# Kernel optimization log

Measured on AMD Instinct MI355X. Metric: run time of the kernel, lower is better.

## Reference

```python
import jax, jax.numpy as jnp
import numpy as np
import math

B, T, C, H, D, R = 1, 2048, 2048, 16, 128, 64
W_LOCAL = 512
DELTA_I = 0.75
ROPE_BASE = 10000.0


def _rotate(x):
    # interleaved rotate-half, exactly as in the torch source
    x1, x2 = x[..., ::2], x[..., 1::2]
    return jnp.stack((-x2, x1), axis=-1).reshape(x.shape)


def _rope_tables(seq_len):
    inv_freq = 1.0 / (ROPE_BASE ** (jnp.arange(0, D, 2, dtype=jnp.float32) / D))
    t = jnp.arange(seq_len, dtype=jnp.float32)
    freqs = jnp.einsum('i,j->ij', t, inv_freq)          # [T, D/2]
    emb = jnp.concatenate((freqs, freqs), axis=-1)      # [T, D] (half-layout, as in source)
    return jnp.cos(emb)[None, None], jnp.sin(emb)[None, None]


def setup_inputs() -> dict:
    key = jax.random.key(0)
    ks = jax.random.split(key, 8)
    s = 0.02
    return {
        'x': jax.random.normal(ks[0], (B, T, C), dtype=jnp.float32),
        'w_qkv': jax.random.normal(ks[1], (3 * C, C), dtype=jnp.float32) * s,
        'w_o': jax.random.normal(ks[2], (C, C), dtype=jnp.float32) * s,
        'pk': jax.random.normal(ks[3], (R, D), dtype=jnp.float32) * s,
        'pv': jax.random.normal(ks[4], (R, D), dtype=jnp.float32) * s,
        'uo': jax.random.normal(ks[5], (D, R), dtype=jnp.float32) * s,
        'info_w1': jax.random.normal(ks[6], (C // 4, C), dtype=jnp.float32) * s,
        'info_w2': jax.random.normal(ks[7], (1, C // 4), dtype=jnp.float32) * s,
    }


def reference(x, w_qkv, w_o, pk, pv, uo, info_w1, info_w2):
    Bx, Tx, Cx = x.shape
    scale = 1.0 / math.sqrt(D)

    qkv = x @ w_qkv.T                                   # [B,T,3C]
    q, k, v = jnp.split(qkv, 3, axis=-1)
    q = q.reshape(Bx, Tx, H, D).transpose(0, 2, 1, 3)   # [B,H,T,D]
    k = k.reshape(Bx, Tx, H, D).transpose(0, 2, 1, 3)
    v = v.reshape(Bx, Tx, H, D).transpose(0, 2, 1, 3)

    cos, sin = _rope_tables(Tx)
    q = q * cos + _rotate(q) * sin
    k = k * cos + _rotate(k) * sin

    # causal local-window attention (full [B,H,T,T] scores, as in source)
    w = min(W_LOCAL, Tx)
    idx = jnp.arange(Tx)
    rel = idx[None, :] - idx[:, None]                   # j - i
    local_mask = (rel > 0) | (rel < -(w - 1))           # True = masked
    scores = jnp.einsum('bhtd,bhsd->bhts', q, k) * scale
    scores = jnp.where(local_mask[None, None], -jnp.inf, scores)
    attn_local = jax.nn.softmax(scores, axis=-1)
    ctx_local = jnp.einsum('bhts,bhsd->bhtd', attn_local, v)

    # informational gate (no-grad path in source)
    h_info = jax.nn.gelu(x @ info_w1.T, approximate=False)
    info_score = jax.nn.sigmoid((h_info @ info_w2.T)[..., 0])   # [B,T]
    gate = (info_score > DELTA_I).astype(x.dtype)

    # low-rank global path (unmasked softmax over all tokens, as in source)
    k_r = jnp.einsum('bhsd,rd->bhsr', k, pk)
    v_r = jnp.einsum('bhsd,rd->bhsr', v, pv)
    q_r = jnp.einsum('bhtd,rd->bhtr', q, pk)
    scores_g = jnp.einsum('bhtr,bhsr->bhts', q_r, k_r) * (scale * D / R)
    attn_g = jax.nn.softmax(scores_g, axis=-1)
    ctx_g_r = jnp.einsum('bhts,bhsr->bhtr', attn_g, v_r)
    ctx_g = jnp.einsum('bhtr,dr->bhtd', ctx_g_r, uo)
    gate_q = gate[:, None, :, None]                     # [B,1,T,1]
    ctx = ctx_local + ctx_g * gate_q

    ctx = ctx.transpose(0, 2, 1, 3).reshape(Bx, Tx, Cx)
    return ctx @ w_o.T
```

## Files before the change

### kernel.cpp

```cpp
#include <hip/hip_runtime.h>
#include <hip/hip_bf16.h>
#include <math.h>

#define T_LEN 2048
#define C_DIM 2048
#define NH 16
#define HD 128
#define RANK 64
#define W_LOCAL 512
#define QKV_LD 6144
#define ROW_BF 12288
#define KB_OFF 4096
#define VB_OFF 8192
#define WO_OFF 6144
#define SCALE 0.08838834764831845f
#define SCALE_G 0.17677669529663687f
#define LOG1E4_OVER_64 0.14391156831212787f

typedef __bf16 bf16_t;
typedef __bf16 bf16x8 __attribute__((ext_vector_type(8)));
typedef __bf16 bf16x4 __attribute__((ext_vector_type(4)));
typedef float f32x4 __attribute__((ext_vector_type(4)));

__device__ __forceinline__ void async_copy16(const bf16_t* g, bf16_t* l) {
    __builtin_amdgcn_global_load_lds(
        (const __attribute__((address_space(1))) unsigned int*)g,
        (__attribute__((address_space(3))) unsigned int*)l, 16, 0, 0);
}

__global__ __launch_bounds__(256)
void prep_kernel(const float* __restrict__ x, bf16_t* __restrict__ xb,
                 const float* __restrict__ w_qkv, bf16_t* __restrict__ wqb,
                 float* __restrict__ tab) {
    const int bid = blockIdx.x;
    const int tid = threadIdx.x;
    if (bid < 2048) {
        int idx = bid * 256 + tid;
        const float* p = x + (size_t)idx * 8;
        float4 v0 = *(const float4*)p;
        float4 v1 = *(const float4*)(p + 4);
        bf16x8 o;
        o[0] = (bf16_t)v0.x; o[1] = (bf16_t)v0.y; o[2] = (bf16_t)v0.z; o[3] = (bf16_t)v0.w;
        o[4] = (bf16_t)v1.x; o[5] = (bf16_t)v1.y; o[6] = (bf16_t)v1.z; o[7] = (bf16_t)v1.w;
        *(bf16x8*)(xb + (size_t)idx * 8) = o;
    } else if (bid < 8192) {
        int idx = (bid - 2048) * 256 + tid;
        const float* p = w_qkv + (size_t)idx * 8;
        float4 v0 = *(const float4*)p;
        float4 v1 = *(const float4*)(p + 4);
        bf16x8 o;
        o[0] = (bf16_t)v0.x; o[1] = (bf16_t)v0.y; o[2] = (bf16_t)v0.z; o[3] = (bf16_t)v0.w;
        o[4] = (bf16_t)v1.x; o[5] = (bf16_t)v1.y; o[6] = (bf16_t)v1.z; o[7] = (bf16_t)v1.w;
        *(bf16x8*)(wqb + (size_t)idx * 8) = o;
    } else {
        int idx = (bid - 8192) * 256 + tid;
        int t = idx >> 6, j = idx & 63;
        float inv = expf(-(float)j * LOG1E4_OVER_64);
        float s, c;
        sincosf((float)t * inv, &s, &c);
        tab[t * 128 + j] = c;
        tab[t * 128 + 64 + j] = s;
    }
}

#define NTK 32
#define ILD 40

#define STG_A(bb, ktile) do {                                                  \
    _Pragma("unroll")                                                          \
    for (int c_ = 0; c_ < 4; ++c_)                                             \
        async_copy16(gA + (size_t)(c_ * 32) * 2048 + (ktile) * 64,             \
                     &lds[bb][0][(c_ * 32 + rS) * 64 + dS]);                   \
} while (0)

#define STG_B(bb, ktile) do {                                                  \
    _Pragma("unroll")                                                          \
    for (int c_ = 0; c_ < 4; ++c_)                                             \
        async_copy16(gB + (size_t)(c_ * 32) * 2048 + (ktile) * 64,             \
                     &lds[bb][1][(c_ * 32 + rS) * 64 + dS]);                   \
} while (0)

#define RD_A(bb, m, k) (*(const bf16x8*)&lds[bb][0][(wr * 64 + (m) * 16 + l16) * 64 + (((k) * 4 + quad) ^ xsw) * 8])
#define RD_B(bb, n, k) (*(const bf16x8*)&lds[bb][1][(wc * 64 + (n) * 16 + l16) * 64 + (((k) * 4 + quad) ^ xsw) * 8])

__global__ __launch_bounds__(256, 2)
void gemm_qkv_rope(const bf16_t* __restrict__ A, const bf16_t* __restrict__ B,
                   bf16_t* __restrict__ qkv_bf, bf16_t* __restrict__ vt,
                   const float* __restrict__ tab, const float* __restrict__ w_o,
                   const float* __restrict__ x, const float* __restrict__ w1,
                   float* __restrict__ ipart) {
    __shared__ __align__(16) unsigned char smem[65536];
    const int bid = blockIdx.x;
    const int tid = threadIdx.x;

    if (bid < 128) {
        bf16_t* Ah = (bf16_t*)smem;
        bf16_t* Al = Ah + 128 * ILD;
        bf16_t* Bh = Al + 128 * ILD;
        bf16_t* Bl = Bh + 128 * ILD;
        const int bn = bid & 3, bm = (bid >> 2) & 15, ks = bid >> 6;
        const int wave = tid >> 6, lane = tid & 63;
        const int quad = lane >> 4, l16 = lane & 15;
        const int wm = (wave >> 1) * 64, wn = (wave & 1) * 64;
        const int lrow = lane >> 2;
        const int lkb = (lane & 3) * 8;
        const int kbeg = ks * 1024;

        f32x4 acc[4][4];
#pragma unroll
        for (int i = 0; i < 4; ++i)
#pragma unroll
            for (int j = 0; j < 4; ++j) acc[i][j] = (f32x4){0.f, 0.f, 0.f, 0.f};

        const float* gx = x + (size_t)(bm * 128 + wave * 16 + lrow) * 2048 + kbeg + lkb;
        const float* gw = w1 + (size_t)(bn * 128 + wave * 16 + lrow) * 2048 + kbeg + lkb;
        const int wrow = (wave * 16 + lrow) * ILD + lkb;

        for (int k0 = 0; k0 < 1024; k0 += 32) {
            __syncthreads();
#pragma unroll
            for (int hr = 0; hr < 2; ++hr) {
                const float* px = gx + (size_t)hr * 64 * 2048 + k0;
                float4 a0 = *(const float4*)px, a1 = *(const float4*)(px + 4);
                float av[8] = {a0.x, a0.y, a0.z, a0.w, a1.x, a1.y, a1.z, a1.w};
                bf16x8 h, l;
#pragma unroll
                for (int i = 0; i < 8; ++i) {
                    bf16_t hb = (bf16_t)av[i];
                    h[i] = hb; l[i] = (bf16_t)(av[i] - (float)hb);
                }
                *(bf16x8*)&Ah[wrow + hr * 64 * ILD] = h;
                *(bf16x8*)&Al[wrow + hr * 64 * ILD] = l;

                const float* pw = gw + (size_t)hr * 64 * 2048 + k0;
                float4 b0 = *(const float4*)pw, b1 = *(const float4*)(pw + 4);
                float bv[8] = {b0.x, b0.y, b0.z, b0.w, b1.x, b1.y, b1.z, b1.w};
                bf16x8 hb2, lb2;
#pragma unroll
                for (int i = 0; i < 8; ++i) {
                    bf16_t hh = (bf16_t)bv[i];
                    hb2[i] = hh; lb2[i] = (bf16_t)(bv[i] - (float)hh);
                }
                *(bf16x8*)&Bh[wrow + hr * 64 * ILD] = hb2;
                *(bf16x8*)&Bl[wrow + hr * 64 * ILD] = lb2;
            }
            __syncthreads();

            bf16x8 ah[4], al[4], bh[4], bl[4];
#pragma unroll
            for (int mt = 0; mt < 4; ++mt) {
                ah[mt] = *(const bf16x8*)&Ah[(wm + mt * 16 + l16) * ILD + quad * 8];
                al[mt] = *(const bf16x8*)&Al[(wm + mt * 16 + l16) * ILD + quad * 8];
            }
#pragma unroll
            for (int nt = 0; nt < 4; ++nt) {
                bh[nt] = *(const bf16x8*)&Bh[(wn + nt * 16 + l16) * ILD + quad * 8];
                bl[nt] = *(const bf16x8*)&Bl[(wn + nt * 16 + l16) * ILD + quad * 8];
            }
#pragma unroll
            for (int mt = 0; mt < 4; ++mt)
#pragma unroll
                for (int nt = 0; nt < 4; ++nt) {
                    acc[mt][nt] = __builtin_amdgcn_mfma_f32_16x16x32_bf16(ah[mt], bh[nt], acc[mt][nt], 0, 0, 0);
                    acc[mt][nt] = __builtin_amdgcn_mfma_f32_16x16x32_bf16(ah[mt], bl[nt], acc[mt][nt], 0, 0, 0);
                    acc[mt][nt] = __builtin_amdgcn_mfma_f32_16x16x32_bf16(al[mt], bh[nt], acc[mt][nt], 0, 0, 0);
                }
        }

        float* cp = ipart + (size_t)ks * 2048 * 512;
#pragma unroll
        for (int mt = 0; mt < 4; ++mt)
#pragma unroll
            for (int r = 0; r < 4; ++r) {
                int row = bm * 128 + wm + mt * 16 + quad * 4 + r;
                float* crow = cp + (size_t)row * 512 + bn * 128 + wn;
#pragma unroll
                for (int nt = 0; nt < 4; ++nt)
                    crow[nt * 16 + l16] = acc[mt][nt][r];
            }
        return;
    }

    if (bid >= 896) {
        int row = bid - 896;
        int c = tid * 8;
        const float* p = w_o + (size_t)row * 2048 + c;
        float4 v0 = *(const float4*)p;
        float4 v1 = *(const float4*)(p + 4);
        bf16x8 o;
        o[0] = (bf16_t)v0.x; o[1] = (bf16_t)v0.y; o[2] = (bf16_t)v0.z; o[3] = (bf16_t)v0.w;
        o[4] = (bf16_t)v1.x; o[5] = (bf16_t)v1.y; o[6] = (bf16_t)v1.z; o[7] = (bf16_t)v1.w;
        *(bf16x8*)(qkv_bf + (size_t)row * ROW_BF + WO_OFF + c) = o;
        return;
    }

    typedef bf16_t ldsbuf_t[2][128 * 64];
    ldsbuf_t* lds = (ldsbuf_t*)smem;

    const int gid = bid - 128;
    const int xcd = gid & 7, idx = gid >> 3;
    const int bn_ = xcd * 6 + (idx >> 4);
    const int bm_ = idx & 15;
    const int wave = tid >> 6, lane = tid & 63;
    const int quad = lane >> 4, l16 = lane & 15;
    const int wr = wave >> 1, wc = wave & 1;
    const int xsw = l16 & 7;

    const int rS = tid >> 3;
    const int cS = ((tid & 7) ^ (rS & 7)) * 8;
    const int dS = (tid & 7) * 8;
    const bf16_t* gA = A + (size_t)(bm_ * 128 + rS) * 2048 + cS;
    const bf16_t* gB = B + (size_t)(bn_ * 128 + rS) * 2048 + cS;

    f32x4 acc[4][4];
#pragma unroll
    for (int i = 0; i < 4; ++i)
#pragma unroll
        for (int j = 0; j < 4; ++j) acc[i][j] = (f32x4){0.f, 0.f, 0.f, 0.f};

    STG_A(0, 0); STG_B(0, 0);
    STG_A(1, 1); STG_B(1, 1);
    asm volatile("s_waitcnt vmcnt(8)" ::: "memory");
    __builtin_amdgcn_s_barrier();

    for (int kt = 0; kt < NTK; ++kt) {
        const int b = kt & 1;
        bf16x8 af[4][2], bfr[4][2];
#pragma unroll
        for (int m = 0; m < 4; ++m) { af[m][0] = RD_A(b, m, 0); af[m][1] = RD_A(b, m, 1); }
#pragma unroll
        for (int n = 0; n < 4; ++n) { bfr[n][0] = RD_B(b, n, 0); bfr[n][1] = RD_B(b, n, 1); }
        asm volatile("s_waitcnt lgkmcnt(0)" ::: "memory");
        __builtin_amdgcn_s_barrier();

        __builtin_amdgcn_s_setprio(1);
#pragma unroll
        for (int m = 0; m < 4; ++m)
#pragma unroll
            for (int n = 0; n < 4; ++n)
                acc[m][n] = __builtin_amdgcn_mfma_f32_16x16x32_bf16(af[m][0], bfr[n][0], acc[m][n], 0, 0, 0);
        __builtin_amdgcn_s_setprio(0);
        if (kt + 2 < NTK) STG_A(b, kt + 2);

        __builtin_amdgcn_s_setprio(1);
#pragma unroll
        for (int m = 0; m < 4; ++m)
#pragma unroll
            for (int n = 0; n < 4; ++n)
                acc[m][n] = __builtin_amdgcn_mfma_f32_16x16x32_bf16(af[m][1], bfr[n][1], acc[m][n], 0, 0, 0);
        __builtin_amdgcn_s_setprio(0);
        if (kt + 2 < NTK) STG_B(b, kt + 2);

        if (kt < NTK - 2) { asm volatile("s_waitcnt vmcnt(8)" ::: "memory"); }
        else              { asm volatile("s_waitcnt vmcnt(0)" ::: "memory"); }
        __builtin_amdgcn_s_barrier();
    }

    const int colbase = bn_ * 128 + wc * 64;
    const int region = (bn_ * 128) >> 11;
    const int rowbase = bm_ * 128 + wr * 64;
    const bool odd = (l16 & 1);

    if (region == 2) {
#pragma unroll
        for (int mt = 0; mt < 4; ++mt)
#pragma unroll
            for (int r = 0; r < 4; ++r) {
                int t = rowbase + mt * 16 + quad * 4 + r;
                bf16_t* brow = qkv_bf + (size_t)t * ROW_BF + VB_OFF + (colbase - 4096);
#pragma unroll
                for (int nt = 0; nt < 4; ++nt)
                    brow[nt * 16 + l16] = (bf16_t)acc[mt][nt][r];
            }
        bf16_t* Tl = (bf16_t*)smem;
#pragma unroll
        for (int mt = 0; mt < 4; ++mt)
#pragma unroll
            for (int r = 0; r < 4; ++r) {
                int rloc = wr * 64 + mt * 16 + quad * 4 + r;
#pragma unroll
                for (int nt = 0; nt < 4; ++nt) {
                    int cloc = wc * 64 + nt * 16 + l16;
                    Tl[cloc * 136 + rloc] = (bf16_t)acc[mt][nt][r];
                }
            }
        __syncthreads();
        const int hh = bn_ - 32;
        const int d = tid >> 1, th = (tid & 1) * 64;
        bf16_t* dst = vt + ((size_t)(hh * 128 + d)) * 2048 + bm_ * 128 + th;
        const bf16_t* srcT = Tl + d * 136 + th;
#pragma unroll
        for (int j = 0; j < 8; ++j)
            *(bf16x8*)(dst + j * 8) = *(const bf16x8*)(srcT + j * 8);
    } else {
#pragma unroll
        for (int mt = 0; mt < 4; ++mt)
#pragma unroll
            for (int r = 0; r < 4; ++r) {
                int t = rowbase + mt * 16 + quad * 4 + r;
                const float* trow = tab + t * 128;
#pragma unroll
                for (int nt = 0; nt < 4; ++nt) {
                    float v = acc[mt][nt][r];
                    float vp = __shfl_xor(v, 1);
                    int col = colbase + nt * 16 + l16;
                    int j = col & 63;
                    float c = trow[j], s = trow[64 + j];
                    float y = odd ? (v * c + vp * s) : (v * c - vp * s);
                    qkv_bf[(size_t)t * ROW_BF + (region == 0 ? col : col + 2048)] = (bf16_t)y;
                }
            }
    }
}

#define STG_A2(bb, ktile) do {                                                 \
    _Pragma("unroll")                                                          \
    for (int c_ = 0; c_ < 4; ++c_)                                             \
        async_copy16(gA + (size_t)(c_ * 32) * 2048 + (ktile) * 64,             \
                     &lds[bb][0][(c_ * 32 + rS) * 64 + dS]);                   \
} while (0)

#define STG_B2(bb, ktile) do {                                                 \
    _Pragma("unroll")                                                          \
    for (int c_ = 0; c_ < 4; ++c_)                                             \
        async_copy16(gB + (size_t)(c_ * 32) * ROW_BF + (ktile) * 64,           \
                     &lds[bb][1][(c_ * 32 + rS) * 64 + dS]);                   \
} while (0)

__global__ __launch_bounds__(256, 2)
void gemm_ctx_wo(const bf16_t* __restrict__ A, const bf16_t* __restrict__ Bov,
                 float* __restrict__ C) {
    __shared__ __align__(16) bf16_t ldss[2][2][128 * 64];
    typedef bf16_t ldsbuf_t[2][128 * 64];
    ldsbuf_t* lds = (ldsbuf_t*)ldss;

    const int bid = blockIdx.x;
    const int xcd = bid & 7, idx = bid >> 3;
    const int bn_ = xcd * 2 + (idx >> 4);
    const int bm_ = idx & 15;
    const int tid = threadIdx.x;
    const int wave = tid >> 6, lane = tid & 63;
    const int quad = lane >> 4, l16 = lane & 15;
    const int wr = wave >> 1, wc = wave & 1;
    const int xsw = l16 & 7;

    const int rS = tid >> 3;
    const int cS = ((tid & 7) ^ (rS & 7)) * 8;
    const int dS = (tid & 7) * 8;
    const bf16_t* gA = A + (size_t)(bm_ * 128 + rS) * 2048 + cS;
    const bf16_t* gB = Bov + (size_t)(bn_ * 128 + rS) * ROW_BF + cS;

    f32x4 acc[4][4];
#pragma unroll
    for (int i = 0; i < 4; ++i)
#pragma unroll
        for (int j = 0; j < 4; ++j) acc[i][j] = (f32x4){0.f, 0.f, 0.f, 0.f};

    STG_A2(0, 0); STG_B2(0, 0);
    STG_A2(1, 1); STG_B2(1, 1);
    asm volatile("s_waitcnt vmcnt(8)" ::: "memory");
    __builtin_amdgcn_s_barrier();

    for (int kt = 0; kt < NTK; ++kt) {
        const int b = kt & 1;
        bf16x8 af[4][2], bfr[4][2];
#pragma unroll
        for (int m = 0; m < 4; ++m) { af[m][0] = RD_A(b, m, 0); af[m][1] = RD_A(b, m, 1); }
#pragma unroll
        for (int n = 0; n < 4; ++n) { bfr[n][0] = RD_B(b, n, 0); bfr[n][1] = RD_B(b, n, 1); }
        asm volatile("s_waitcnt lgkmcnt(0)" ::: "memory");
        __builtin_amdgcn_s_barrier();

        __builtin_amdgcn_s_setprio(1);
#pragma unroll
        for (int m = 0; m < 4; ++m)
#pragma unroll
            for (int n = 0; n < 4; ++n)
                acc[m][n] = __builtin_amdgcn_mfma_f32_16x16x32_bf16(af[m][0], bfr[n][0], acc[m][n], 0, 0, 0);
        __builtin_amdgcn_s_setprio(0);
        if (kt + 2 < NTK) STG_A2(b, kt + 2);

        __builtin_amdgcn_s_setprio(1);
#pragma unroll
        for (int m = 0; m < 4; ++m)
#pragma unroll
            for (int n = 0; n < 4; ++n)
                acc[m][n] = __builtin_amdgcn_mfma_f32_16x16x32_bf16(af[m][1], bfr[n][1], acc[m][n], 0, 0, 0);
        __builtin_amdgcn_s_setprio(0);
        if (kt + 2 < NTK) STG_B2(b, kt + 2);

        if (kt < NTK - 2) { asm volatile("s_waitcnt vmcnt(8)" ::: "memory"); }
        else              { asm volatile("s_waitcnt vmcnt(0)" ::: "memory"); }
        __builtin_amdgcn_s_barrier();
    }

    const int colbase = bn_ * 128 + wc * 64;
    const int rowbase = bm_ * 128 + wr * 64;
#pragma unroll
    for (int mt = 0; mt < 4; ++mt)
#pragma unroll
        for (int r = 0; r < 4; ++r) {
            int row = rowbase + mt * 16 + quad * 4 + r;
            float* crow = C + (size_t)row * 2048 + colbase;
#pragma unroll
            for (int nt = 0; nt < 4; ++nt)
                crow[nt * 16 + l16] = acc[mt][nt][r];
        }
}

__device__ __forceinline__ float gelu_exact(float v) {
    return 0.5f * v * (1.0f + erff(v * 0.70710678118654752f));
}

__global__ __launch_bounds__(64)
void info_gate_kernel(const float* __restrict__ Cpart, const float* __restrict__ w2,
                      float* __restrict__ gate) {
    const int t = blockIdx.x;
    const int lane = threadIdx.x;
    const float* p0 = Cpart + (size_t)t * 512;
    float s = 0.f;
#pragma unroll
    for (int i = lane; i < 512; i += 64) {
        float v = p0[i] + p0[i + 1048576];
        s += gelu_exact(v) * w2[i];
    }
#pragma unroll
    for (int off = 32; off > 0; off >>= 1) s += __shfl_down(s, off);
    if (lane == 0) {
        float sig = 1.f / (1.f + expf(-s));
        gate[t] = (sig > 0.75f) ? 1.f : 0.f;
    }
}

#define KV_LD 136

__global__ __launch_bounds__(256)
void kvr_mfma_kernel(const bf16_t* __restrict__ qkv_bf,
                     const float* __restrict__ pk, const float* __restrict__ pv,
                     float* __restrict__ kr, float* __restrict__ vr,
                     bf16_t* __restrict__ qr) {
    __shared__ bf16_t Kt[64 * KV_LD];
    __shared__ bf16_t Vt[64 * KV_LD];
    __shared__ bf16_t Qt[64 * KV_LD];
    __shared__ bf16_t Pk[64 * KV_LD];
    __shared__ bf16_t Pv[64 * KV_LD];

    const int h = blockIdx.y;
    const int s0 = blockIdx.x * 64;
    const int tid = threadIdx.x;
    const int wave = tid >> 6, lane = tid & 63;
    const int quad = lane >> 4, l16 = lane & 15;

#pragma unroll
    for (int i = 0; i < 4; ++i) {
        int gid = i * 256 + tid;
        int row = gid >> 4, ch = (gid & 15) << 3;
        const bf16_t* rb = qkv_bf + (size_t)(s0 + row) * ROW_BF + h * HD + ch;
        *(bf16x8*)&Qt[row * KV_LD + ch] = *(const bf16x8*)(rb);
        *(bf16x8*)&Kt[row * KV_LD + ch] = *(const bf16x8*)(rb + KB_OFF);
        *(bf16x8*)&Vt[row * KV_LD + ch] = *(const bf16x8*)(rb + VB_OFF);
    }
#pragma unroll
    for (int i = 0; i < 8; ++i) {
        int gid = i * 256 + tid;
        int row = gid >> 5, c = (gid & 31) << 2;
        float4 wk = *(const float4*)(pk + (size_t)row * HD + c);
        float4 wv = *(const float4*)(pv + (size_t)row * HD + c);
        bf16x4 qk4, qv4;
        qk4[0] = (bf16_t)wk.x; qk4[1] = (bf16_t)wk.y; qk4[2] = (bf16_t)wk.z; qk4[3] = (bf16_t)wk.w;
        qv4[0] = (bf16_t)wv.x; qv4[1] = (bf16_t)wv.y; qv4[2] = (bf16_t)wv.z; qv4[3] = (bf16_t)wv.w;
        *(bf16x4*)&Pk[row * KV_LD + c] = qk4;
        *(bf16x4*)&Pv[row * KV_LD + c] = qv4;
    }
    __syncthreads();

    f32x4 ak[4], av[4], aq[4];
#pragma unroll
    for (int nt = 0; nt < 4; ++nt) {
        ak[nt] = (f32x4){0.f, 0.f, 0.f, 0.f};
        av[nt] = (f32x4){0.f, 0.f, 0.f, 0.f};
        aq[nt] = (f32x4){0.f, 0.f, 0.f, 0.f};
    }

#pragma unroll
    for (int ks = 0; ks < 4; ++ks) {
        const int ao = (wave * 16 + l16) * KV_LD + ks * 32 + quad * 8;
        bf16x8 a_k = *(const bf16x8*)&Kt[ao];
        bf16x8 a_v = *(const bf16x8*)&Vt[ao];
        bf16x8 a_q = *(const bf16x8*)&Qt[ao];
#pragma unroll
        for (int nt = 0; nt < 4; ++nt) {
            const int bo = (nt * 16 + l16) * KV_LD + ks * 32 + quad * 8;
            bf16x8 bk = *(const bf16x8*)&Pk[bo];
            bf16x8 bv = *(const bf16x8*)&Pv[bo];
            ak[nt] = __builtin_amdgcn_mfma_f32_16x16x32_bf16(a_k, bk, ak[nt], 0, 0, 0);
            av[nt] = __builtin_amdgcn_mfma_f32_16x16x32_bf16(a_v, bv, av[nt], 0, 0, 0);
            aq[nt] = __builtin_amdgcn_mfma_f32_16x16x32_bf16(a_q, bk, aq[nt], 0, 0, 0);
        }
    }

#pragma unroll
    for (int nt = 0; nt < 4; ++nt)
#pragma unroll
        for (int r = 0; r < 4; ++r) {
            int s = s0 + wave * 16 + quad * 4 + r;
            size_t idx = ((size_t)h * T_LEN + s) * RANK + nt * 16 + l16;
            kr[idx] = ak[nt][r];
            vr[idx] = av[nt][r];
            qr[idx] = (bf16_t)aq[nt][r];
        }
}

#define QTI 64
#define KTI 64
#define PS_LD 72

__global__ __launch_bounds__(256)
void local_attn_kernel(const bf16_t* __restrict__ qkv_bf, const bf16_t* __restrict__ vt,
                       bf16_t* __restrict__ cxb) {
    __shared__ __align__(16) bf16_t Qs[QTI * 128];
    __shared__ __align__(16) bf16_t Ks[KTI * 128];
    __shared__ __align__(16) bf16_t Vts[128 * KTI];
    __shared__ bf16_t Ps[4][16 * PS_LD];

    const int h = blockIdx.y;
    const int t0 = blockIdx.x * QTI;
    const int tid = threadIdx.x;
    const int wave = tid >> 6, lane = tid & 63;
    const int quad = lane >> 4, l16 = lane & 15;
    const int xsw = l16 & 7;

    const bf16_t* vth = vt + (size_t)h * 128 * 2048;

#pragma unroll
    for (int i = 0; i < 4; ++i) {
        int c = i * 256 + tid;
        int row = c >> 4, pc = c & 15;
        int lc = pc ^ (row & 7);
        async_copy16(qkv_bf + (size_t)(t0 + row) * ROW_BF + h * HD + lc * 8, &Qs[c * 8]);
    }

    f32x4 o[8];
#pragma unroll
    for (int d8 = 0; d8 < 8; ++d8) o[d8] = (f32x4){0.f, 0.f, 0.f, 0.f};
    float m_i[4] = {-1e30f, -1e30f, -1e30f, -1e30f};
    float l_i[4] = {0.f, 0.f, 0.f, 0.f};

    __syncthreads();

    for (int kt = 0; kt < 9; ++kt) {
        const int sbase = t0 - 512 + kt * KTI;
        if (sbase < 0) continue;
        __syncthreads();
#pragma unroll
        for (int i = 0; i < 4; ++i) {
            int c = i * 256 + tid;
            int row = c >> 4, pc = c & 15;
            int lc = pc ^ (row & 7);
            async_copy16(qkv_bf + (size_t)(sbase + row) * ROW_BF + KB_OFF + h * HD + lc * 8,
                         &Ks[c * 8]);
        }
#pragma unroll
        for (int i = 0; i < 4; ++i) {
            int c = i * 256 + tid;
            int row = c >> 3, pc = c & 7;
            int lc = pc ^ (row & 7);
            async_copy16(vth + (size_t)row * 2048 + sbase + lc * 8, &Vts[c * 8]);
        }
        __syncthreads();

        f32x4 sacc[4];
#pragma unroll
        for (int nt = 0; nt < 4; ++nt) sacc[nt] = (f32x4){0.f, 0.f, 0.f, 0.f};
#pragma unroll
        for (int ks = 0; ks < 4; ++ks) {
            bf16x8 a = *(const bf16x8*)&Qs[(wave * 16 + l16) * 128 + (((ks * 4 + quad) ^ xsw)) * 8];
#pragma unroll
            for (int nt = 0; nt < 4; ++nt) {
                bf16x8 b = *(const bf16x8*)&Ks[(nt * 16 + l16) * 128 + (((ks * 4 + quad) ^ xsw)) * 8];
                sacc[nt] = __builtin_amdgcn_mfma_f32_16x16x32_bf16(a, b, sacc[nt], 0, 0, 0);
            }
        }

#pragma unroll
        for (int nt = 0; nt < 4; ++nt)
#pragma unroll
            for (int r = 0; r < 4; ++r) sacc[nt][r] *= SCALE;

        if (kt == 0 || kt == 8) {
#pragma unroll
            for (int nt = 0; nt < 4; ++nt) {
                int s_g = sbase + nt * 16 + l16;
#pragma unroll
                for (int r = 0; r < 4; ++r) {
                    int t_g = t0 + wave * 16 + quad * 4 + r;
                    bool valid = (s_g <= t_g) && (s_g + W_LOCAL > t_g);
                    if (!valid) sacc[nt][r] = -1e30f;
                }
            }
        }

#pragma unroll
        for (int r = 0; r < 4; ++r) {
            float mx = fmaxf(fmaxf(sacc[0][r], sacc[1][r]), fmaxf(sacc[2][r], sacc[3][r]));
            mx = fmaxf(mx, __shfl_xor(mx, 1));
            mx = fmaxf(mx, __shfl_xor(mx, 2));
            mx = fmaxf(mx, __shfl_xor(mx, 4));
            mx = fmaxf(mx, __shfl_xor(mx, 8));
            float mnew = fmaxf(m_i[r], mx);
            float alpha = __expf(m_i[r] - mnew);
            m_i[r] = mnew;
            float rs = 0.f;
#pragma unroll
            for (int nt = 0; nt < 4; ++nt) {
                float p = __expf(sacc[nt][r] - mnew);
                sacc[nt][r] = p;
                rs += p;
            }
            rs += __shfl_xor(rs, 1);
            rs += __shfl_xor(rs, 2);
            rs += __shfl_xor(rs, 4);
            rs += __shfl_xor(rs, 8);
            l_i[r] = l_i[r] * alpha + rs;
#pragma unroll
            for (int d8 = 0; d8 < 8; ++d8) o[d8][r] *= alpha;
        }

#pragma unroll
        for (int r = 0; r < 4; ++r)
#pragma unroll
            for (int nt = 0; nt < 4; ++nt)
                Ps[wave][(quad * 4 + r) * PS_LD + nt * 16 + l16] = (bf16_t)sacc[nt][r];

#pragma unroll
        for (int ks2 = 0; ks2 < 2; ++ks2) {
            bf16x8 a = *(const bf16x8*)&Ps[wave][l16 * PS_LD + ks2 * 32 + quad * 8];
#pragma unroll
            for (int d8 = 0; d8 < 8; ++d8) {
                int rw = d8 * 16 + l16;
                bf16x8 b = *(const bf16x8*)&Vts[rw * 64 + (((ks2 * 4 + quad) ^ xsw)) * 8];
                o[d8] = __builtin_amdgcn_mfma_f32_16x16x32_bf16(a, b, o[d8], 0, 0, 0);
            }
        }
    }

#pragma unroll
    for (int r = 0; r < 4; ++r) {
        float inv = 1.0f / l_i[r];
        size_t rowoff = (size_t)(t0 + wave * 16 + quad * 4 + r) * 2048 + h * HD;
#pragma unroll
        for (int d8 = 0; d8 < 8; ++d8)
            cxb[rowoff + d8 * 16 + l16] = (bf16_t)(o[d8][r] * inv);
    }
}

__device__ __forceinline__ float block_reduce_max512(float v, float* red, int tid) {
    red[tid] = v; __syncthreads();
    for (int s = 256; s > 0; s >>= 1) {
        if (tid < s) red[tid] = fmaxf(red[tid], red[tid + s]);
        __syncthreads();
    }
    float r = red[0]; __syncthreads();
    return r;
}
__device__ __forceinline__ float block_reduce_sum512(float v, float* red, int tid) {
    red[tid] = v; __syncthreads();
    for (int s = 256; s > 0; s >>= 1) {
        if (tid < s) red[tid] = red[tid] + red[tid + s];
        __syncthreads();
    }
    float r = red[0]; __syncthreads();
    return r;
}

__global__ __launch_bounds__(512)
void global_attn_kernel(bf16_t* __restrict__ cxb, const float* __restrict__ kr,
                        const float* __restrict__ vr, const bf16_t* __restrict__ qr,
                        const float* __restrict__ uo, const float* __restrict__ gate) {
    const int t = blockIdx.x, h = blockIdx.y;
    if (gate[t] <= 0.5f) return;

    __shared__ float qrs[64];
    __shared__ float red[512];
    __shared__ float cgr[64];
    __shared__ float sg[2048];
    const int tid = threadIdx.x;

    if (tid < 64) qrs[tid] = (float)qr[((size_t)h * T_LEN + t) * RANK + tid];
    __syncthreads();

    const float* krh = kr + (size_t)h * T_LEN * RANK;
    const float* vrh = vr + (size_t)h * T_LEN * RANK;
    float lmax = -INFINITY;
    for (int s = tid; s < T_LEN; s += 512) {
        const float* krr = krh + (size_t)s * RANK;
        float acc = 0.f;
#pragma unroll
        for (int r = 0; r < RANK; r += 4) {
            float4 k4 = *(const float4*)(krr + r);
            acc += qrs[r] * k4.x + qrs[r + 1] * k4.y + qrs[r + 2] * k4.z + qrs[r + 3] * k4.w;
        }
        float sc = acc * SCALE_G;
        sg[s] = sc;
        lmax = fmaxf(lmax, sc);
    }
    float gmx = block_reduce_max512(lmax, red, tid);
    float lsum = 0.f;
    for (int s = tid; s < T_LEN; s += 512) {
        float pp = expf(sg[s] - gmx);
        sg[s] = pp;
        lsum += pp;
    }
    float gsum = block_reduce_sum512(lsum, red, tid);

    {
        const int r = tid & 63, part = tid >> 6;
        float pacc = 0.f;
        for (int s = part; s < T_LEN; s += 8) pacc += sg[s] * vrh[(size_t)s * RANK + r];
        red[tid] = pacc;
        __syncthreads();
        if (tid < 64) {
            float c = 0.f;
#pragma unroll
            for (int pp = 0; pp < 8; ++pp) c += red[pp * 64 + tid];
            cgr[tid] = c / gsum;
        }
        __syncthreads();
    }

    if (tid < 128) {
        float cg = 0.f;
#pragma unroll
        for (int r = 0; r < RANK; ++r) cg += cgr[r] * uo[tid * RANK + r];
        size_t off = (size_t)t * 2048 + h * HD + tid;
        cxb[off] = (bf16_t)((float)cxb[off] + cg);
    }
}

extern "C" void kernel_launch(void* const* d_in, const int* in_sizes, int n_in,
                              void* d_out, int out_size, void* d_ws, size_t ws_size,
                              hipStream_t stream) {
    const float* x     = (const float*)d_in[0];
    const float* w_qkv = (const float*)d_in[1];
    const float* w_o   = (const float*)d_in[2];
    const float* pk    = (const float*)d_in[3];
    const float* pv    = (const float*)d_in[4];
    const float* uo    = (const float*)d_in[5];
    const float* w1    = (const float*)d_in[6];
    const float* w2    = (const float*)d_in[7];
    float* out = (float*)d_out;

    float* ws = (float*)d_ws;
    float* qkv   = ws;
    float* hinfo = qkv + (size_t)12582912;
    float* gatep = hinfo + (size_t)1048576;
    bf16_t* xb   = (bf16_t*)(gatep + 2048);
    float* wqbf  = gatep + 2048 + 2097152;
    bf16_t* wqb  = (bf16_t*)wqbf;
    float* krp   = wqbf;
    float* vrp   = wqbf + (size_t)2097152;
    float* tabp  = hinfo;
    bf16_t* qrp  = (bf16_t*)hinfo;
    bf16_t* cxb  = xb;
    bf16_t* qkvb = (bf16_t*)qkv;
    bf16_t* wob  = qkvb + WO_OFF;
    bf16_t* vtp  = (bf16_t*)d_out;
    float* ipart = (float*)(vtp + (size_t)16 * 128 * 2048);

    prep_kernel<<<8704, 256, 0, stream>>>(x, xb, w_qkv, wqb, tabp);
    gemm_qkv_rope<<<2944, 256, 0, stream>>>(xb, wqb, qkvb, vtp, tabp, w_o, x, w1, ipart);
    info_gate_kernel<<<T_LEN, 64, 0, stream>>>(ipart, w2, gatep);
    kvr_mfma_kernel<<<dim3(T_LEN / 64, NH), 256, 0, stream>>>(qkvb, pk, pv, krp, vrp, qrp);
    local_attn_kernel<<<dim3(T_LEN / QTI, NH), 256, 0, stream>>>(qkvb, vtp, cxb);
    global_attn_kernel<<<dim3(T_LEN, NH), 512, 0, stream>>>(cxb, krp, vrp, qrp, uo, gatep);
    gemm_ctx_wo<<<256, 256, 0, stream>>>(cxb, wob, out);
}
```

Baseline: 294.0 us.

## Fuse info gate, low-rank projection and local attention into one launch; shrink out-proj tile

Merges the info-gate, K/V/Q rank-projection and local-attention kernels into a single launch that branches on block index, so the three independent stages share one grid and skip two launch boundaries. The projection branch now stages K, V and Q through one reused LDS buffer in turn to cut LDS use, which adds extra barriers. Separately, the output-projection GEMM tile narrows from 128x128 to 128x64 and the grid doubles to 512 blocks for better CU coverage, at the cost of less data reuse per block.

```diff
diff --git a/kernel.cpp b/kernel.cpp
--- a/kernel.cpp
+++ b/kernel.cpp
@@ -313,30 +313,32 @@
     }
 }
 
-#define STG_A2(bb, ktile) do {                                                 \
+#define STG_A3(bb, ktile) do {                                                 \
     _Pragma("unroll")                                                          \
     for (int c_ = 0; c_ < 4; ++c_)                                             \
         async_copy16(gA + (size_t)(c_ * 32) * 2048 + (ktile) * 64,             \
-                     &lds[bb][0][(c_ * 32 + rS) * 64 + dS]);                   \
+                     &ldsA[bb][(c_ * 32 + rS) * 64 + dS]);                     \
 } while (0)
 
-#define STG_B2(bb, ktile) do {                                                 \
+#define STG_B3(bb, ktile) do {                                                 \
     _Pragma("unroll")                                                          \
-    for (int c_ = 0; c_ < 4; ++c_)                                             \
+    for (int c_ = 0; c_ < 2; ++c_)                                             \
         async_copy16(gB + (size_t)(c_ * 32) * ROW_BF + (ktile) * 64,           \
-                     &lds[bb][1][(c_ * 32 + rS) * 64 + dS]);                   \
+                     &ldsB[bb][(c_ * 32 + rS) * 64 + dS]);                     \
 } while (0)
+
+#define RD_A3(bb, m, k) (*(const bf16x8*)&ldsA[bb][(wr * 64 + (m) * 16 + l16) * 64 + (((k) * 4 + quad) ^ xsw) * 8])
+#define RD_B3(bb, n, k) (*(const bf16x8*)&ldsB[bb][(wc * 32 + (n) * 16 + l16) * 64 + (((k) * 4 + quad) ^ xsw) * 8])
 
 __global__ __launch_bounds__(256, 2)
 void gemm_ctx_wo(const bf16_t* __restrict__ A, const bf16_t* __restrict__ Bov,
                  float* __restrict__ C) {
-    __shared__ __align__(16) bf16_t ldss[2][2][128 * 64];
-    typedef bf16_t ldsbuf_t[2][128 * 64];
-    ldsbuf_t* lds = (ldsbuf_t*)ldss;
+    __shared__ __align__(16) bf16_t ldsA[2][128 * 64];
+    __shared__ __align__(16) bf16_t ldsB[2][64 * 64];
 
     const int bid = blockIdx.x;
     const int xcd = bid & 7, idx = bid >> 3;
-    const int bn_ = xcd * 2 + (idx >> 4);
+    const int bn_ = xcd * 4 + (idx >> 4);
     const int bm_ = idx & 15;
     const int tid = threadIdx.x;
     const int wave = tid >> 6, lane = tid & 63;
@@ -348,26 +350,26 @@
     const int cS = ((tid & 7) ^ (rS & 7)) * 8;
     const int dS = (tid & 7) * 8;
     const bf16_t* gA = A + (size_t)(bm_ * 128 + rS) * 2048 + cS;
-    const bf16_t* gB = Bov + (size_t)(bn_ * 128 + rS) * ROW_BF + cS;
-
-    f32x4 acc[4][4];
+    const bf16_t* gB = Bov + (size_t)(bn_ * 64 + rS) * ROW_BF + cS;
+
+    f32x4 acc[4][2];
 #pragma unroll
     for (int i = 0; i < 4; ++i)
 #pragma unroll
-        for (int j = 0; j < 4; ++j) acc[i][j] = (f32x4){0.f, 0.f, 0.f, 0.f};
-
-    STG_A2(0, 0); STG_B2(0, 0);
-    STG_A2(1, 1); STG_B2(1, 1);
-    asm volatile("s_waitcnt vmcnt(8)" ::: "memory");
+        for (int j = 0; j < 2; ++j) acc[i][j] = (f32x4){0.f, 0.f, 0.f, 0.f};
+
+    STG_A3(0, 0); STG_B3(0, 0);
+    STG_A3(1, 1); STG_B3(1, 1);
+    asm volatile("s_waitcnt vmcnt(6)" ::: "memory");
     __builtin_amdgcn_s_barrier();
 
     for (int kt = 0; kt < NTK; ++kt) {
         const int b = kt & 1;
-        bf16x8 af[4][2], bfr[4][2];
-#pragma unroll
-        for (int m = 0; m < 4; ++m) { af[m][0] = RD_A(b, m, 0); af[m][1] = RD_A(b, m, 1); }
-#pragma unroll
-        for (int n = 0; n < 4; ++n) { bfr[n][0] = RD_B(b, n, 0); bfr[n][1] = RD_B(b, n, 1); }
+        bf16x8 af[4][2], bfr[2][2];
+#pragma unroll
+        for (int m = 0; m < 4; ++m) { af[m][0] = RD_A3(b, m, 0); af[m][1] = RD_A3(b, m, 1); }
+#pragma unroll
+        for (int n = 0; n < 2; ++n) { bfr[n][0] = RD_B3(b, n, 0); bfr[n][1] = RD_B3(b, n, 1); }
         asm volatile("s_waitcnt lgkmcnt(0)" ::: "memory");
         __builtin_amdgcn_s_barrier();
 
@@ -375,26 +377,26 @@
 #pragma unroll
         for (int m = 0; m < 4; ++m)
 #pragma unroll
-            for (int n = 0; n < 4; ++n)
+            for (int n = 0; n < 2; ++n)
                 acc[m][n] = __builtin_amdgcn_mfma_f32_16x16x32_bf16(af[m][0], bfr[n][0], acc[m][n], 0, 0, 0);
         __builtin_amdgcn_s_setprio(0);
-        if (kt + 2 < NTK) STG_A2(b, kt + 2);
+        if (kt + 2 < NTK) STG_A3(b, kt + 2);
 
         __builtin_amdgcn_s_setprio(1);
 #pragma unroll
         for (int m = 0; m < 4; ++m)
 #pragma unroll
-            for (int n = 0; n < 4; ++n)
+            for (int n = 0; n < 2; ++n)
                 acc[m][n] = __builtin_amdgcn_mfma_f32_16x16x32_bf16(af[m][1], bfr[n][1], acc[m][n], 0, 0, 0);
         __builtin_amdgcn_s_setprio(0);
-        if (kt + 2 < NTK) STG_B2(b, kt + 2);
-
-        if (kt < NTK - 2) { asm volatile("s_waitcnt vmcnt(8)" ::: "memory"); }
+        if (kt + 2 < NTK) STG_B3(b, kt + 2);
+
+        if (kt < NTK - 2) { asm volatile("s_waitcnt vmcnt(6)" ::: "memory"); }
         else              { asm volatile("s_waitcnt vmcnt(0)" ::: "memory"); }
         __builtin_amdgcn_s_barrier();
     }
 
-    const int colbase = bn_ * 128 + wc * 64;
+    const int colbase = bn_ * 64 + wc * 32;
     const int rowbase = bm_ * 128 + wr * 64;
 #pragma unroll
     for (int mt = 0; mt < 4; ++mt)
@@ -403,7 +405,7 @@
             int row = rowbase + mt * 16 + quad * 4 + r;
             float* crow = C + (size_t)row * 2048 + colbase;
 #pragma unroll
-            for (int nt = 0; nt < 4; ++nt)
+            for (int nt = 0; nt < 2; ++nt)
                 crow[nt * 16 + l16] = acc[mt][nt][r];
         }
 }
@@ -412,122 +414,145 @@
     return 0.5f * v * (1.0f + erff(v * 0.70710678118654752f));
 }
 
-__global__ __launch_bounds__(64)
-void info_gate_kernel(const float* __restrict__ Cpart, const float* __restrict__ w2,
-                      float* __restrict__ gate) {
-    const int t = blockIdx.x;
-    const int lane = threadIdx.x;
-    const float* p0 = Cpart + (size_t)t * 512;
-    float s = 0.f;
-#pragma unroll
-    for (int i = lane; i < 512; i += 64) {
-        float v = p0[i] + p0[i + 1048576];
-        s += gelu_exact(v) * w2[i];
-    }
-#pragma unroll
-    for (int off = 32; off > 0; off >>= 1) s += __shfl_down(s, off);
-    if (lane == 0) {
-        float sig = 1.f / (1.f + expf(-s));
-        gate[t] = (sig > 0.75f) ? 1.f : 0.f;
-    }
-}
-
+#define QTI 64
+#define KTI 64
+#define PS_LD 72
 #define KV_LD 136
 
-__global__ __launch_bounds__(256)
-void kvr_mfma_kernel(const bf16_t* __restrict__ qkv_bf,
-                     const float* __restrict__ pk, const float* __restrict__ pv,
-                     float* __restrict__ kr, float* __restrict__ vr,
-                     bf16_t* __restrict__ qr) {
-    __shared__ bf16_t Kt[64 * KV_LD];
-    __shared__ bf16_t Vt[64 * KV_LD];
-    __shared__ bf16_t Qt[64 * KV_LD];
-    __shared__ bf16_t Pk[64 * KV_LD];
-    __shared__ bf16_t Pv[64 * KV_LD];
-
-    const int h = blockIdx.y;
-    const int s0 = blockIdx.x * 64;
+__global__ __launch_bounds__(256, 2)
+void attn_fused(const bf16_t* __restrict__ qkv_bf, const bf16_t* __restrict__ vt,
+                bf16_t* __restrict__ cxb,
+                const float* __restrict__ pk, const float* __restrict__ pv,
+                float* __restrict__ kr, float* __restrict__ vr,
+                bf16_t* __restrict__ qr,
+                const float* __restrict__ Cpart, const float* __restrict__ w2,
+                float* __restrict__ gate) {
+    __shared__ __align__(16) unsigned char smem[58368];
+    const int bid = blockIdx.x;
     const int tid = threadIdx.x;
     const int wave = tid >> 6, lane = tid & 63;
     const int quad = lane >> 4, l16 = lane & 15;
 
-#pragma unroll
-    for (int i = 0; i < 4; ++i) {
-        int gid = i * 256 + tid;
-        int row = gid >> 4, ch = (gid & 15) << 3;
-        const bf16_t* rb = qkv_bf + (size_t)(s0 + row) * ROW_BF + h * HD + ch;
-        *(bf16x8*)&Qt[row * KV_LD + ch] = *(const bf16x8*)(rb);
-        *(bf16x8*)&Kt[row * KV_LD + ch] = *(const bf16x8*)(rb + KB_OFF);
-        *(bf16x8*)&Vt[row * KV_LD + ch] = *(const bf16x8*)(rb + VB_OFF);
-    }
-#pragma unroll
-    for (int i = 0; i < 8; ++i) {
-        int gid = i * 256 + tid;
-        int row = gid >> 5, c = (gid & 31) << 2;
-        float4 wk = *(const float4*)(pk + (size_t)row * HD + c);
-        float4 wv = *(const float4*)(pv + (size_t)row * HD + c);
-        bf16x4 qk4, qv4;
-        qk4[0] = (bf16_t)wk.x; qk4[1] = (bf16_t)wk.y; qk4[2] = (bf16_t)wk.z; qk4[3] = (bf16_t)wk.w;
-        qv4[0] = (bf16_t)wv.x; qv4[1] = (bf16_t)wv.y; qv4[2] = (bf16_t)wv.z; qv4[3] = (bf16_t)wv.w;
-        *(bf16x4*)&Pk[row * KV_LD + c] = qk4;
-        *(bf16x4*)&Pv[row * KV_LD + c] = qv4;
-    }
-    __syncthreads();
-
-    f32x4 ak[4], av[4], aq[4];
-#pragma unroll
-    for (int nt = 0; nt < 4; ++nt) {
-        ak[nt] = (f32x4){0.f, 0.f, 0.f, 0.f};
-        av[nt] = (f32x4){0.f, 0.f, 0.f, 0.f};
-        aq[nt] = (f32x4){0.f, 0.f, 0.f, 0.f};
-    }
-
-#pragma unroll
-    for (int ks = 0; ks < 4; ++ks) {
-        const int ao = (wave * 16 + l16) * KV_LD + ks * 32 + quad * 8;
-        bf16x8 a_k = *(const bf16x8*)&Kt[ao];
-        bf16x8 a_v = *(const bf16x8*)&Vt[ao];
-        bf16x8 a_q = *(const bf16x8*)&Qt[ao];
+    if (bid >= 1024) {
+        const int t = (bid - 1024) * 4 + wave;
+        const float* p0 = Cpart + (size_t)t * 512;
+        float s = 0.f;
+#pragma unroll
+        for (int i = lane; i < 512; i += 64) {
+            float v = p0[i] + p0[i + 1048576];
+            s += gelu_exact(v) * w2[i];
+        }
+#pragma unroll
+        for (int off = 32; off > 0; off >>= 1) s += __shfl_down(s, off);
+        if (lane == 0) {
+            float sig = 1.f / (1.f + expf(-s));
+            gate[t] = (sig > 0.75f) ? 1.f : 0.f;
+        }
+        return;
+    }
+
+    if (bid >= 512) {
+        bf16_t* Pk = (bf16_t*)smem;
+        bf16_t* Pv = Pk + 64 * KV_LD;
+        bf16_t* Op = Pv + 64 * KV_LD;
+        const int i0 = bid - 512;
+        const int h = i0 >> 5, s0 = (i0 & 31) * 64;
+
+#pragma unroll
+        for (int i = 0; i < 8; ++i) {
+            int gid = i * 256 + tid;
+            int row = gid >> 5, c = (gid & 31) << 2;
+            float4 wk = *(const float4*)(pk + (size_t)row * HD + c);
+            float4 wv = *(const float4*)(pv + (size_t)row * HD + c);
+            bf16x4 qk4, qv4;
+            qk4[0] = (bf16_t)wk.x; qk4[1] = (bf16_t)wk.y; qk4[2] = (bf16_t)wk.z; qk4[3] = (bf16_t)wk.w;
+            qv4[0] = (bf16_t)wv.x; qv4[1] = (bf16_t)wv.y; qv4[2] = (bf16_t)wv.z; qv4[3] = (bf16_t)wv.w;
+            *(bf16x4*)&Pk[row * KV_LD + c] = qk4;
+            *(bf16x4*)&Pv[row * KV_LD + c] = qv4;
+        }
+
+        f32x4 ak[4], av[4], aq[4];
 #pragma unroll
         for (int nt = 0; nt < 4; ++nt) {
-            const int bo = (nt * 16 + l16) * KV_LD + ks * 32 + quad * 8;
-            bf16x8 bk = *(const bf16x8*)&Pk[bo];
-            bf16x8 bv = *(const bf16x8*)&Pv[bo];
-            ak[nt] = __builtin_amdgcn_mfma_f32_16x16x32_bf16(a_k, bk, ak[nt], 0, 0, 0);
-            av[nt] = __builtin_amdgcn_mfma_f32_16x16x32_bf16(a_v, bv, av[nt], 0, 0, 0);
-            aq[nt] = __builtin_amdgcn_mfma_f32_16x16x32_bf16(a_q, bk, aq[nt], 0, 0, 0);
-        }
-    }
-
-#pragma unroll
-    for (int nt = 0; nt < 4; ++nt)
-#pragma unroll
-        for (int r = 0; r < 4; ++r) {
-            int s = s0 + wave * 16 + quad * 4 + r;
-            size_t idx = ((size_t)h * T_LEN + s) * RANK + nt * 16 + l16;
-            kr[idx] = ak[nt][r];
-            vr[idx] = av[nt][r];
-            qr[idx] = (bf16_t)aq[nt][r];
-        }
-}
-
-#define QTI 64
-#define KTI 64
-#define PS_LD 72
-
-__global__ __launch_bounds__(256)
-void local_attn_kernel(const bf16_t* __restrict__ qkv_bf, const bf16_t* __restrict__ vt,
-                       bf16_t* __restrict__ cxb) {
-    __shared__ __align__(16) bf16_t Qs[QTI * 128];
-    __shared__ __align__(16) bf16_t Ks[KTI * 128];
-    __shared__ __align__(16) bf16_t Vts[128 * KTI];
-    __shared__ bf16_t Ps[4][16 * PS_LD];
-
-    const int h = blockIdx.y;
-    const int t0 = blockIdx.x * QTI;
-    const int tid = threadIdx.x;
-    const int wave = tid >> 6, lane = tid & 63;
-    const int quad = lane >> 4, l16 = lane & 15;
+            ak[nt] = (f32x4){0.f, 0.f, 0.f, 0.f};
+            av[nt] = (f32x4){0.f, 0.f, 0.f, 0.f};
+            aq[nt] = (f32x4){0.f, 0.f, 0.f, 0.f};
+        }
+
+#pragma unroll
+        for (int i = 0; i < 4; ++i) {
+            int gid = i * 256 + tid;
+            int row = gid >> 4, ch = (gid & 15) << 3;
+            *(bf16x8*)&Op[row * KV_LD + ch] =
+                *(const bf16x8*)(qkv_bf + (size_t)(s0 + row) * ROW_BF + KB_OFF + h * HD + ch);
+        }
+        __syncthreads();
+#pragma unroll
+        for (int ks = 0; ks < 4; ++ks) {
+            bf16x8 a = *(const bf16x8*)&Op[(wave * 16 + l16) * KV_LD + ks * 32 + quad * 8];
+#pragma unroll
+            for (int nt = 0; nt < 4; ++nt) {
+                bf16x8 bk = *(const bf16x8*)&Pk[(nt * 16 + l16) * KV_LD + ks * 32 + quad * 8];
+                ak[nt] = __builtin_amdgcn_mfma_f32_16x16x32_bf16(a, bk, ak[nt], 0, 0, 0);
+            }
+        }
+        __syncthreads();
+#pragma unroll
+        for (int i = 0; i < 4; ++i) {
+            int gid = i * 256 + tid;
+            int row = gid >> 4, ch = (gid & 15) << 3;
+            *(bf16x8*)&Op[row * KV_LD + ch] =
+                *(const bf16x8*)(qkv_bf + (size_t)(s0 + row) * ROW_BF + VB_OFF + h * HD + ch);
+        }
+        __syncthreads();
+#pragma unroll
+        for (int ks = 0; ks < 4; ++ks) {
+            bf16x8 a = *(const bf16x8*)&Op[(wave * 16 + l16) * KV_LD + ks * 32 + quad * 8];
+#pragma unroll
+            for (int nt = 0; nt < 4; ++nt) {
+                bf16x8 bv = *(const bf16x8*)&Pv[(nt * 16 + l16) * KV_LD + ks * 32 + quad * 8];
+                av[nt] = __builtin_amdgcn_mfma_f32_16x16x32_bf16(a, bv, av[nt], 0, 0, 0);
+            }
+        }
+        __syncthreads();
+#pragma unroll
+        for (int i = 0; i < 4; ++i) {
+            int gid = i * 256 + tid;
+            int row = gid >> 4, ch = (gid & 15) << 3;
+            *(bf16x8*)&Op[row * KV_LD + ch] =
+                *(const bf16x8*)(qkv_bf + (size_t)(s0 + row) * ROW_BF + h * HD + ch);
+        }
+        __syncthreads();
+#pragma unroll
+        for (int ks = 0; ks < 4; ++ks) {
+            bf16x8 a = *(const bf16x8*)&Op[(wave * 16 + l16) * KV_LD + ks * 32 + quad * 8];
+#pragma unroll
+            for (int nt = 0; nt < 4; ++nt) {
+                bf16x8 bk = *(const bf16x8*)&Pk[(nt * 16 + l16) * KV_LD + ks * 32 + quad * 8];
+                aq[nt] = __builtin_amdgcn_mfma_f32_16x16x32_bf16(a, bk, aq[nt], 0, 0, 0);
+            }
+        }
+
+#pragma unroll
+        for (int nt = 0; nt < 4; ++nt)
+#pragma unroll
+            for (int r = 0; r < 4; ++r) {
+                int s = s0 + wave * 16 + quad * 4 + r;
+                size_t idx = ((size_t)h * T_LEN + s) * RANK + nt * 16 + l16;
+                kr[idx] = ak[nt][r];
+                vr[idx] = av[nt][r];
+                qr[idx] = (bf16_t)aq[nt][r];
+            }
+        return;
+    }
+
+    bf16_t* Qs  = (bf16_t*)smem;
+    bf16_t* Ks  = Qs + QTI * 128;
+    bf16_t* Vts = Ks + KTI * 128;
+    bf16_t* Psb = Vts + 128 * KTI;
+
+    const int h = bid >> 5;
+    const int t0 = (bid & 31) * QTI;
     const int xsw = l16 & 7;
 
     const bf16_t* vth = vt + (size_t)h * 128 * 2048;
@@ -630,11 +655,11 @@
         for (int r = 0; r < 4; ++r)
 #pragma unroll
             for (int nt = 0; nt < 4; ++nt)
-                Ps[wave][(quad * 4 + r) * PS_LD + nt * 16 + l16] = (bf16_t)sacc[nt][r];
+                Psb[wave * 16 * PS_LD + (quad * 4 + r) * PS_LD + nt * 16 + l16] = (bf16_t)sacc[nt][r];
 
 #pragma unroll
         for (int ks2 = 0; ks2 < 2; ++ks2) {
-            bf16x8 a = *(const bf16x8*)&Ps[wave][l16 * PS_LD + ks2 * 32 + quad * 8];
+            bf16x8 a = *(const bf16x8*)&Psb[wave * 16 * PS_LD + l16 * PS_LD + ks2 * 32 + quad * 8];
 #pragma unroll
             for (int d8 = 0; d8 < 8; ++d8) {
                 int rw = d8 * 16 + l16;
@@ -769,9 +794,8 @@
 
     prep_kernel<<<8704, 256, 0, stream>>>(x, xb, w_qkv, wqb, tabp);
     gemm_qkv_rope<<<2944, 256, 0, stream>>>(xb, wqb, qkvb, vtp, tabp, w_o, x, w1, ipart);
-    info_gate_kernel<<<T_LEN, 64, 0, stream>>>(ipart, w2, gatep);
-    kvr_mfma_kernel<<<dim3(T_LEN / 64, NH), 256, 0, stream>>>(qkvb, pk, pv, krp, vrp, qrp);
-    local_attn_kernel<<<dim3(T_LEN / QTI, NH), 256, 0, stream>>>(qkvb, vtp, cxb);
+    attn_fused<<<1536, 256, 0, stream>>>(qkvb, vtp, cxb, pk, pv, krp, vrp, qrp,
+                                         ipart, w2, gatep);
     global_attn_kernel<<<dim3(T_LEN, NH), 512, 0, stream>>>(cxb, krp, vrp, qrp, uo, gatep);
-    gemm_ctx_wo<<<256, 256, 0, stream>>>(cxb, wob, out);
-}
+    gemm_ctx_wo<<<512, 256, 0, stream>>>(cxb, wob, out);
+}
```

Result: faster. 285.8 us (-2.8%).
